# Kernel optimization log

Hardware: AMD Instinct MI355X
Metric: run time of the kernel (lower is better)

## Reference

```python
import jax, jax.numpy as jnp
import numpy as np

L_IN, L_FREQ, L_OUT = 128, 64, 64
C_IN, C_OUT, T_DIM = 64, 64, 256
SPIN = 1

# ---------- self-contained spin-weighted SHT (MW sampling), replacing s2fft ----------

def _mw_thetas(L, extended):
    n = 2 * L - 1 if extended else L
    return (2 * np.arange(n) + 1) * np.pi / (2 * L - 1)

def _wigner_d_stack(L, thetas, n):
    # d^l_{m,n}(theta) = <l,m| exp(-i theta Jy) |l,n>, computed via eigh of the
    # Hermitian angular-momentum operator Jy. Output (ntheta, L, 2L-1), m at col L-1+m.
    nth = len(thetas)
    out = np.zeros((nth, L, 2 * L - 1), dtype=np.float64)
    for l in range(abs(n), L):
        dim = 2 * l + 1
        m = np.arange(-l, l).astype(np.float64)
        ap = np.sqrt(l * (l + 1.0) - m * (m + 1.0))
        Jy = np.zeros((dim, dim), dtype=np.complex128)
        i = np.arange(dim - 1)
        Jy[i + 1, i] = -0.5j * ap
        Jy[i, i + 1] = 0.5j * ap
        lam, V = np.linalg.eigh(Jy)
        coeff = V * np.conj(V[l + n, :])[None, :]
        phases = np.exp(-1j * np.outer(lam, thetas))
        out[:, l, L - 1 - l:L + l] = (coeff @ phases).T.real
    return out

def _mw_quad_weights(L):
    # per-theta weights on the mirror-extended grid: q_t = (1/(2L-1)) sum_k w(k) e^{ik theta_t}
    # with w(k) = int_0^pi e^{ik t} sin(t) dt
    k = np.arange(-(L - 1), L)
    den = np.where(np.abs(k) == 1, 1, 1 - k * k).astype(np.float64)
    w = np.where(k % 2 == 0, 2.0 / den, 0.0).astype(np.complex128)
    w[k == 1] = 0.5j * np.pi
    w[k == -1] = -0.5j * np.pi
    th = _mw_thetas(L, True)
    return ((w[None, :] * np.exp(1j * np.outer(th, k))).sum(1) / (2 * L - 1)).real

# transform kernels are constants (built once at import, numpy)
_D_FWD = jnp.asarray(_wigner_d_stack(L_IN, _mw_thetas(L_IN, True), -SPIN) * _mw_quad_weights(L_IN)[:, None, None], jnp.float32)
_D_INV = jnp.asarray(_wigner_d_stack(L_OUT, _mw_thetas(L_OUT, False), -SPIN), jnp.float32)
_CL_IN = jnp.asarray(((-1.0) ** SPIN) * np.sqrt((2 * np.arange(L_IN) + 1) / (4 * np.pi)), jnp.float32)
_CL_OUT = jnp.asarray(((-1.0) ** SPIN) * np.sqrt((2 * np.arange(L_OUT) + 1) / (4 * np.pi)), jnp.float32)
_m_all = np.arange(-(L_IN - 1), L_IN)
_PARITY = jnp.asarray(np.where((_m_all + SPIN) % 2 == 0, 1.0, -1.0), jnp.float32)

def sht_forward(x):
    # x: (L_IN, 2*L_IN-1, C) real spatial -> flm: (L_IN, 2*L_IN-1, C) complex, m at L_IN-1+m
    nphi = 2 * L_IN - 1
    ftm = jnp.fft.fftshift(jnp.fft.fft(x, axis=1), axes=1) * (2 * jnp.pi / nphi)
    # mirror extension in theta with (-1)^(m+spin) parity (all channels at once)
    g_ext = jnp.concatenate([ftm, _PARITY[None, :, None] * ftm[::-1][1:]], axis=0)
    flm = jnp.einsum('tlm,tmc->lmc', _D_FWD, g_ext)
    return flm * _CL_IN[:, None, None]

def sht_inverse(flm):
    # flm: (L_OUT, 2*L_OUT-1, C) complex -> (L_OUT, 2*L_OUT-1, C) real spatial
    ftm = jnp.einsum('tlm,lmc->tmc', _D_INV, flm * _CL_OUT[:, None, None])
    return (jnp.fft.ifft(jnp.fft.ifftshift(ftm, axes=1), axis=1) * (2 * L_OUT - 1)).real

def resize_flm(flm, l_in, l_out):
    # centered truncation / zero-pad of (L, 2L-1, C) harmonic coefficients
    if l_out <= l_in:
        d = l_in - l_out
        return flm[:l_out, d:d + 2 * l_out - 1]
    d = l_out - l_in
    return jnp.pad(flm, ((0, d), (d, d), (0, 0)))

# ---------- inputs and parameters ----------

def setup_inputs():
    key = jax.random.key(0)
    ks = jax.random.split(key, 12)
    n = lambda i, shape, s: jax.random.normal(ks[i], shape, jnp.float32) * s
    return {
        'x': jax.random.normal(ks[0], (L_IN, 2 * L_IN - 1, C_IN), jnp.float32),
        't_emb': jax.random.normal(ks[1], (T_DIM,), jnp.float32),
        'spec_conv_w': n(2, (C_IN, C_OUT), (1.0 / C_IN) ** 0.5),
        'spec_conv_b': jnp.zeros((C_OUT,), jnp.float32),
        'spec_wr': n(3, (L_FREQ, C_IN, C_OUT), (0.5 / C_IN) ** 0.5),
        'spec_wi': n(4, (L_FREQ, C_IN, C_OUT), (0.5 / C_IN) ** 0.5),
        'spec_tr_w': n(5, (T_DIM, L_FREQ), (1.0 / T_DIM) ** 0.5),
        'spec_tr_b': jnp.zeros((L_FREQ,), jnp.float32),
        'spec_ti_w': n(6, (T_DIM, L_FREQ), (1.0 / T_DIM) ** 0.5),
        'spec_ti_b': jnp.zeros((L_FREQ,), jnp.float32),
        'spat_conv1_w': n(7, (C_IN, C_OUT), (1.0 / C_IN) ** 0.5),
        'spat_conv1_b': jnp.zeros((C_OUT,), jnp.float32),
        'spat_t_w': n(8, (T_DIM, 2 * C_OUT), (1.0 / T_DIM) ** 0.5),
        'spat_t_b': jnp.zeros((2 * C_OUT,), jnp.float32),
        'spat_weight': n(9, (C_OUT, C_OUT), 0.01),
        'spat_conv2_w': n(10, (C_OUT, C_OUT), (1.0 / C_OUT) ** 0.5),
        'spat_conv2_b': jnp.zeros((C_OUT,), jnp.float32),
        'ln_scale': jnp.ones((C_OUT,), jnp.float32),
        'ln_bias': jnp.zeros((C_OUT,), jnp.float32),
    }

def reference(x, t_emb, spec_conv_w, spec_conv_b, spec_wr, spec_wi, spec_tr_w, spec_tr_b, spec_ti_w, spec_ti_b, spat_conv1_w, spat_conv1_b, spat_t_w, spat_t_b, spat_weight, spat_conv2_w, spat_conv2_b, ln_scale, ln_bias):
    # ----- SphericalSpectralTimeConv branch -----
    flm = sht_forward(x)                                   # (L_IN, 2L_IN-1, C_IN) complex
    flm = resize_flm(flm, L_IN, L_FREQ)                    # (L_FREQ, 2L_FREQ-1, C_IN)
    conv_flm = jnp.einsum('lmi,io->lmo', flm, spec_conv_w) + spec_conv_b
    t_c = (t_emb @ spec_tr_w + spec_tr_b) + 1j * (t_emb @ spec_ti_w + spec_ti_b)   # (L_FREQ,)
    w = t_c[:, None, None] * (spec_wr + 1j * spec_wi)      # (L_FREQ, C_IN, C_OUT)
    flm = jnp.einsum('lmi,lio->lmo', flm, w) + conv_flm
    xs = sht_inverse(resize_flm(flm, L_FREQ, L_OUT))       # (L_OUT, 2L_OUT-1, C_OUT) real
    xs = xs / (jnp.linalg.norm(xs, axis=-1, keepdims=True) + 1e-6)
    # ----- SpatialTimeConv branch (path='down') -----
    h = jnp.einsum('lmi,io->lmo', x, spat_conv1_w) + spat_conv1_b
    t = t_emb @ spat_t_w + spat_t_b
    w_t, b_t = t[:C_OUT], t[C_OUT:]
    h = jnp.einsum('lmi,io->lmo', h, w_t[None, :] * spat_weight)
    h = sht_inverse(resize_flm(sht_forward(h), L_IN, L_OUT))
    h = jnp.einsum('lmi,io->lmo', h, spat_conv2_w) + spat_conv2_b + b_t
    # ----- combine: add, gelu, LayerNorm (eps=1e-6 over channels) -----
    y = jax.nn.gelu(xs + h)
    mu = jnp.mean(y, axis=-1, keepdims=True)
    var = jnp.var(y, axis=-1, keepdims=True)
    return (y - mu) * jax.lax.rsqrt(var + 1e-6) * ln_scale + ln_bias
```

## Files before the change

kernel.cpp:

```cpp
#include <hip/hip_runtime.h>
#include <math.h>

#define DPI 3.141592653589793238462643383279502884

__device__ __forceinline__ float wave_sum64(float v) {
#pragma unroll
  for (int off = 32; off > 0; off >>= 1) v += __shfl_xor(v, off, 64);
  return v;
}

__device__ __forceinline__ float gelu_tanh(float v) {
  float u = 0.7978845608028654f * (v + 0.044715f * v * v * v);
  return 0.5f * v * (1.0f + tanhf(u));
}

__global__ __launch_bounds__(256) void ct_setup(
    float* __restrict__ Deff, float* __restrict__ Dinv,
    float2* __restrict__ T255, float2* __restrict__ T127,
    const float* __restrict__ temb, const float* __restrict__ trw,
    const float* __restrict__ trb, const float* __restrict__ tiw,
    const float* __restrict__ tib, const float* __restrict__ stw,
    const float* __restrict__ stb, float* tcr, float* tci, float* tv) {
  int b = blockIdx.x;
  int tid = threadIdx.x;
  if (b >= 255) {
    if (b == 445) {
      if (tid < 64) {
        float ar = trb[tid], ai = tib[tid];
        for (int k = 0; k < 256; ++k) {
          float e = temb[k];
          ar = fmaf(e, trw[k * 64 + tid], ar);
          ai = fmaf(e, tiw[k * 64 + tid], ai);
        }
        tcr[tid] = ar; tci[tid] = ai;
      } else if (tid < 192) {
        int j = tid - 64;
        float a = stb[j];
        for (int k = 0; k < 256; ++k) a = fmaf(temb[k], stw[k * 128 + j], a);
        tv[j] = a;
      }
    } else {
      int id = (b - 255) * 256 + tid;
      if (id < 255 * 127) {
        int p = id / 127, mm = id % 127;
        double ang = 2.0 * DPI * (double)((mm - 63) * p) / 255.0;
        T255[id] = make_float2((float)cos(ang), (float)(-sin(ang)));
      }
      if (id < 127 * 127) {
        int mm = id / 127, p = id % 127;
        double ang = 2.0 * DPI * (double)((mm - 63) * p) / 127.0;
        T127[id] = make_float2((float)cos(ang), (float)sin(ang));
      }
    }
    return;
  }
  __shared__ double red[64];
  __shared__ float clf[64];
  int mode = (b < 128) ? 0 : 1;
  if (tid < 64)
    clf[tid] = (float)(-sqrt((2.0 * tid + 1.0) / (4.0 * DPI)));
  int t, mm;
  if (mode == 0) { t = b; mm = tid; }
  else { mm = b - 128; t = tid; }
  double denomN = (mode == 0) ? 255.0 : 127.0;
  double beta = (2.0 * t + 1.0) * DPI / denomN;
  float coeff;
  if (mode == 0) {
    if (tid < 63) {
      int k = 2 * (tid + 1);
      red[tid] = 8.0 * cos((double)k * beta) / (1.0 - (double)k * (double)k);
    } else if (tid == 63) {
      red[63] = 4.0;
    }
    __syncthreads();
    for (int s = 32; s > 0; s >>= 1) {
      if (tid < s) red[tid] += red[tid + s];
      __syncthreads();
    }
    double s = red[0] / 255.0;
    if (t == 127) s *= 0.5;
    coeff = (float)(s * (2.0 * DPI / 255.0));
    if (tid >= 127) return;
  } else {
    __syncthreads();
    coeff = 1.0f;
    if (tid >= 64) return;
  }
  int m = mm - 63;
  double cb = cos(beta);
  double ch = cos(0.5 * beta), sh = sin(0.5 * beta);
  int am = (m < 0) ? -m : m;
  int l0v = (am > 1) ? am : 1;
  double seed;
  if (m >= 1) {
    double j = (double)m;
    double K = exp(0.5 * (lgamma(2.0 * j + 1.0) - lgamma(j) - lgamma(j + 2.0)));
    double sgn = ((m + 1) & 1) ? -1.0 : 1.0;
    seed = sgn * K * pow(ch, j - 1.0) * pow(sh, j + 1.0);
  } else if (m <= -1) {
    double j = (double)(-m);
    double K = exp(0.5 * (lgamma(2.0 * j + 1.0) - lgamma(j) - lgamma(j + 2.0)));
    seed = K * pow(ch, j + 1.0) * pow(sh, j - 1.0);
  } else {
    seed = -sqrt(2.0) * sh * ch;
  }
  float dl = (float)seed, dm1 = 0.0f, S_cur = 0.0f;
  float cbf = (float)cb, mf = (float)m;
  for (int l = 0; l < 64; ++l) {
    float val = 0.0f;
    if (l >= l0v) {
      val = dl * coeff * clf[l];
      float Ld = (float)l, lp = Ld + 1.0f;
      float S_next = sqrtf((lp * lp - mf * mf) * (lp * lp - 1.0f));
      float num1 = (2.0f * Ld + 1.0f) * (Ld * lp * cbf + mf);
      float dn = (num1 * dl - lp * S_cur * dm1) / (Ld * S_next);
      dm1 = dl; dl = dn; S_cur = S_next;
    }
    if (mode == 0) Deff[((size_t)t * 127 + mm) * 64 + l] = val;
    else Dinv[((size_t)mm * 64 + l) * 64 + t] = val;
  }
}

__global__ void ct_AM(const float* __restrict__ cw, const float* __restrict__ wr,
                      const float* __restrict__ wi, const float* __restrict__ tcr,
                      const float* __restrict__ tci, const float* __restrict__ c1w,
                      const float* __restrict__ c1b, const float* __restrict__ sw,
                      const float* __restrict__ tv, const float* __restrict__ Deff,
                      float2* __restrict__ A2, float* __restrict__ Mm,
                      float* __restrict__ bias2, float* __restrict__ Sl) {
  int b = blockIdx.x, o = threadIdx.x;
  if (b < 64) {
    int l = b;
    float tr = tcr[l], ti = tci[l];
    for (int i = 0; i < 64; ++i) {
      int idx = (l * 64 + i) * 64 + o;
      float r = wr[idx], s = wi[idx];
      A2[idx] = make_float2(cw[i * 64 + o] + tr * r - ti * s, tr * s + ti * r);
    }
  } else if (b < 128) {
    int j = b - 64;
    float wt = tv[o];
    float acc = 0.f;
    for (int i = 0; i < 64; ++i) acc = fmaf(c1w[j * 64 + i], sw[i * 64 + o], acc);
    Mm[j * 64 + o] = wt * acc;
    if (j == 0) {
      float bb = 0.f;
      for (int i = 0; i < 64; ++i) bb = fmaf(c1b[i], sw[i * 64 + o], bb);
      bias2[o] = wt * bb;
    }
  } else {
    int l = o;
    float s = 0.f;
    for (int t = 0; t < 128; ++t) s += Deff[((size_t)t * 127 + 63) * 64 + l];
    Sl[l] = s;
  }
}

__global__ __launch_bounds__(256) void ct_dft(const float* __restrict__ x,
                                              const float2* __restrict__ T255,
                                              float* __restrict__ Are, float* __restrict__ Aim,
                                              float* __restrict__ Bre, float* __restrict__ Bim) {
  __shared__ float xs_[64][64];
  __shared__ float tsr[64][64], tsi[64][64];
  int t = blockIdx.x, mh = blockIdx.y, ph = blockIdx.z;
  float* ore = ph ? Bre : Are;
  float* oim = ph ? Bim : Aim;
  int pbase = ph * 128;
  int Ktot = ph ? 127 : 128;
  int tid = threadIdx.x;
  int cg = tid & 15, mg = tid >> 4;
  float accr[4][4], acci[4][4];
#pragma unroll
  for (int j = 0; j < 4; ++j)
#pragma unroll
    for (int q = 0; q < 4; ++q) { accr[j][q] = 0.f; acci[j][q] = 0.f; }
  for (int k0 = 0; k0 < Ktot; k0 += 64) {
    int kn = (Ktot - k0 < 64) ? Ktot - k0 : 64;
    __syncthreads();
    {
      int r = tid >> 2, c4 = (tid & 3) * 16;
      if (r < kn) {
        const float4* src = (const float4*)(x + ((size_t)t * 255 + pbase + k0 + r) * 64 + c4);
        float4* dst = (float4*)&xs_[r][c4];
        dst[0] = src[0]; dst[1] = src[1]; dst[2] = src[2]; dst[3] = src[3];
      }
    }
    for (int e = tid; e < 64 * 64; e += 256) {
      int r = e >> 6, mi = e & 63;
      if (r < kn) {
        int gcol = mh * 64 + mi; if (gcol > 126) gcol = 126;
        float2 tw = T255[(size_t)(pbase + k0 + r) * 127 + gcol];
        tsr[r][mi] = tw.x; tsi[r][mi] = tw.y;
      }
    }
    __syncthreads();
#pragma unroll 4
    for (int k = 0; k < kn; ++k) {
      float4 xv = *(const float4*)&xs_[k][cg * 4];
      float4 tr4 = *(const float4*)&tsr[k][mg * 4];
      float4 ti4 = *(const float4*)&tsi[k][mg * 4];
      float xv4[4] = {xv.x, xv.y, xv.z, xv.w};
      float trv[4] = {tr4.x, tr4.y, tr4.z, tr4.w};
      float tiv[4] = {ti4.x, ti4.y, ti4.z, ti4.w};
#pragma unroll
      for (int j = 0; j < 4; ++j)
#pragma unroll
        for (int q = 0; q < 4; ++q) {
          accr[j][q] = fmaf(xv4[q], trv[j], accr[j][q]);
          acci[j][q] = fmaf(xv4[q], tiv[j], acci[j][q]);
        }
    }
  }
#pragma unroll
  for (int j = 0; j < 4; ++j) {
    int gmm = mh * 64 + mg * 4 + j;
    if (gmm > 126) continue;
    size_t ob = ((size_t)t * 127 + gmm) * 64 + cg * 4;
    *(float4*)(ore + ob) = make_float4(accr[j][0], accr[j][1], accr[j][2], accr[j][3]);
    *(float4*)(oim + ob) = make_float4(acci[j][0], acci[j][1], acci[j][2], acci[j][3]);
  }
}

__global__ __launch_bounds__(256) void ct_projf(const float* __restrict__ Deff,
                                                const float* __restrict__ fAre,
                                                const float* __restrict__ fAim,
                                                const float* __restrict__ fBre,
                                                const float* __restrict__ fBim,
                                                float* __restrict__ flmA_re, float* __restrict__ flmA_im,
                                                float* __restrict__ flmB_re, float* __restrict__ flmB_im) {
  __shared__ float Dsh[64][32];
  __shared__ float fr_[64][64], fi_[64][64];
  int mm = blockIdx.x, lh = blockIdx.y, th = blockIdx.z;
  float* ore = th ? flmB_re : flmA_re;
  float* oim = th ? flmB_im : flmA_im;
  int tb = th * 64;
  int tid = threadIdx.x;
  int cg = tid & 15, lg = tid >> 4;
  for (int e = tid; e < 64 * 32; e += 256) {
    int r = e >> 5, li = e & 31;
    Dsh[r][li] = Deff[((size_t)(tb + r) * 127 + mm) * 64 + lh * 32 + li];
  }
  for (int e = tid; e < 64 * 64; e += 256) {
    int r = e >> 6, c = e & 63;
    size_t idx = ((size_t)(tb + r) * 127 + mm) * 64 + c;
    fr_[r][c] = fAre[idx] + fBre[idx];
    fi_[r][c] = fAim[idx] + fBim[idx];
  }
  __syncthreads();
  float ar[2][4], ai[2][4];
#pragma unroll
  for (int li = 0; li < 2; ++li)
#pragma unroll
    for (int q = 0; q < 4; ++q) { ar[li][q] = 0.f; ai[li][q] = 0.f; }
#pragma unroll 4
  for (int k = 0; k < 64; ++k) {
    float4 fr4 = *(const float4*)&fr_[k][cg * 4];
    float4 fi4 = *(const float4*)&fi_[k][cg * 4];
    float2 d2 = *(const float2*)&Dsh[k][lg * 2];
    float frv[4] = {fr4.x, fr4.y, fr4.z, fr4.w};
    float fiv[4] = {fi4.x, fi4.y, fi4.z, fi4.w};
    float dv[2] = {d2.x, d2.y};
#pragma unroll
    for (int li = 0; li < 2; ++li)
#pragma unroll
      for (int q = 0; q < 4; ++q) {
        ar[li][q] = fmaf(dv[li], frv[q], ar[li][q]);
        ai[li][q] = fmaf(dv[li], fiv[q], ai[li][q]);
      }
  }
#pragma unroll
  for (int li = 0; li < 2; ++li) {
    size_t row = ((size_t)mm * 64 + lh * 32 + lg * 2 + li) * 64 + cg * 4;
    *(float4*)(ore + row) = make_float4(ar[li][0], ar[li][1], ar[li][2], ar[li][3]);
    *(float4*)(oim + row) = make_float4(ai[li][0], ai[li][1], ai[li][2], ai[li][3]);
  }
}

__global__ __launch_bounds__(256) void ct_mix(const float* __restrict__ flmA_re,
                                              const float* __restrict__ flmA_im,
                                              const float* __restrict__ flmB_re,
                                              const float* __restrict__ flmB_im,
                                              const float2* __restrict__ A2,
                                              const float* __restrict__ Mm,
                                              const float* __restrict__ scb,
                                              const float* __restrict__ bias2,
                                              const float* __restrict__ Sl,
                                              float* __restrict__ s_re, float* __restrict__ s_im,
                                              float* __restrict__ h_re, float* __restrict__ h_im) {
  __shared__ float Ar_[64][32], Ai_[64][32], Msh[64][32];
  __shared__ float Br_[64][65], Bi_[64][65];
  int l = blockIdx.x, mh = blockIdx.y, oh = blockIdx.z;
  int tid = threadIdx.x;
  int og = tid & 15, mg = tid >> 4;
  for (int e = tid; e < 64 * 32; e += 256) {
    int r = e >> 5, oi = e & 31;
    float2 a = A2[((size_t)l * 64 + r) * 64 + oh * 32 + oi];
    Ar_[r][oi] = a.x; Ai_[r][oi] = a.y;
    Msh[r][oi] = Mm[r * 64 + oh * 32 + oi];
  }
  for (int e = tid; e < 64 * 64; e += 256) {
    int mi = e >> 6, i = e & 63;
    int gmm = mh * 64 + mi; if (gmm > 126) gmm = 126;
    size_t idx = ((size_t)gmm * 64 + l) * 64 + i;
    Br_[mi][i] = flmA_re[idx] + flmB_re[idx];
    Bi_[mi][i] = flmA_im[idx] + flmB_im[idx];
  }
  __syncthreads();
  int o0 = oh * 32 + og * 2;
  float b0[2] = {scb[o0], scb[o0 + 1]};
  float sr[4][2], si[4][2], hr[4][2], hi[4][2];
#pragma unroll
  for (int jm = 0; jm < 4; ++jm)
#pragma unroll
    for (int qo = 0; qo < 2; ++qo) {
      sr[jm][qo] = b0[qo]; si[jm][qo] = 0.f; hr[jm][qo] = 0.f; hi[jm][qo] = 0.f;
    }
#pragma unroll 4
  for (int k = 0; k < 64; ++k) {
    float2 ar2 = *(const float2*)&Ar_[k][og * 2];
    float2 ai2 = *(const float2*)&Ai_[k][og * 2];
    float2 mv2 = *(const float2*)&Msh[k][og * 2];
    float br4[4], bi4[4];
#pragma unroll
    for (int jm = 0; jm < 4; ++jm) {
      br4[jm] = Br_[mg * 4 + jm][k];
      bi4[jm] = Bi_[mg * 4 + jm][k];
    }
    float arv[2] = {ar2.x, ar2.y}, aiv[2] = {ai2.x, ai2.y}, mvv[2] = {mv2.x, mv2.y};
#pragma unroll
    for (int jm = 0; jm < 4; ++jm)
#pragma unroll
      for (int qo = 0; qo < 2; ++qo) {
        sr[jm][qo] = fmaf(br4[jm], arv[qo], sr[jm][qo]);
        sr[jm][qo] = fmaf(-bi4[jm], aiv[qo], sr[jm][qo]);
        si[jm][qo] = fmaf(br4[jm], aiv[qo], si[jm][qo]);
        si[jm][qo] = fmaf(bi4[jm], arv[qo], si[jm][qo]);
        hr[jm][qo] = fmaf(br4[jm], mvv[qo], hr[jm][qo]);
        hi[jm][qo] = fmaf(bi4[jm], mvv[qo], hi[jm][qo]);
      }
  }
  float Slv = Sl[l];
  float bb[2] = {bias2[o0], bias2[o0 + 1]};
#pragma unroll
  for (int jm = 0; jm < 4; ++jm) {
    int gmm = mh * 64 + mg * 4 + jm;
    if (gmm > 126) continue;
    if (gmm == 63) {
#pragma unroll
      for (int qo = 0; qo < 2; ++qo)
        hr[jm][qo] = fmaf(255.0f * Slv, bb[qo], hr[jm][qo]);
    }
    size_t row = ((size_t)gmm * 64 + l) * 64 + o0;
    *(float2*)(s_re + row) = make_float2(sr[jm][0], sr[jm][1]);
    *(float2*)(s_im + row) = make_float2(si[jm][0], si[jm][1]);
    *(float2*)(h_re + row) = make_float2(hr[jm][0], hr[jm][1]);
    *(float2*)(h_im + row) = make_float2(hi[jm][0], hi[jm][1]);
  }
}

__global__ __launch_bounds__(256) void ct_proji(const float* __restrict__ Dinv,
                                                const float* __restrict__ s_re,
                                                const float* __restrict__ s_im,
                                                const float* __restrict__ h_re,
                                                const float* __restrict__ h_im,
                                                float* __restrict__ fos_re, float* __restrict__ fos_im,
                                                float* __restrict__ foh_re, float* __restrict__ foh_im) {
  __shared__ float Dsh[64][64];
  __shared__ float Br_[64][32], Bi_[64][32];
  int mm = blockIdx.x, br = blockIdx.y, ch = blockIdx.z;
  const float* ire = br ? h_re : s_re;
  const float* iim = br ? h_im : s_im;
  float* ore = br ? foh_re : fos_re;
  float* oim = br ? foh_im : fos_im;
  int tid = threadIdx.x;
  int cg = tid & 15, tg = tid >> 4;
  for (int e = tid; e < 64 * 64; e += 256) {
    int r = e >> 6, tt = e & 63;
    Dsh[r][tt] = Dinv[((size_t)mm * 64 + r) * 64 + tt];
  }
  for (int e = tid; e < 64 * 32; e += 256) {
    int r = e >> 5, cc = e & 31;
    size_t idx = ((size_t)mm * 64 + r) * 64 + ch * 32 + cc;
    Br_[r][cc] = ire[idx];
    Bi_[r][cc] = iim[idx];
  }
  __syncthreads();
  float ar[4][2], ai[4][2];
#pragma unroll
  for (int j = 0; j < 4; ++j)
#pragma unroll
    for (int q = 0; q < 2; ++q) { ar[j][q] = 0.f; ai[j][q] = 0.f; }
#pragma unroll 4
  for (int k = 0; k < 64; ++k) {
    float4 d4 = *(const float4*)&Dsh[k][tg * 4];
    float2 fr2 = *(const float2*)&Br_[k][cg * 2];
    float2 fi2 = *(const float2*)&Bi_[k][cg * 2];
    float dv[4] = {d4.x, d4.y, d4.z, d4.w};
    float frv[2] = {fr2.x, fr2.y}, fiv[2] = {fi2.x, fi2.y};
#pragma unroll
    for (int j = 0; j < 4; ++j)
#pragma unroll
      for (int q = 0; q < 2; ++q) {
        ar[j][q] = fmaf(dv[j], frv[q], ar[j][q]);
        ai[j][q] = fmaf(dv[j], fiv[q], ai[j][q]);
      }
  }
#pragma unroll
  for (int j = 0; j < 4; ++j) {
    int t = tg * 4 + j;
    size_t ob = ((size_t)t * 127 + mm) * 64 + ch * 32 + cg * 2;
    *(float2*)(ore + ob) = make_float2(ar[j][0], ar[j][1]);
    *(float2*)(oim + ob) = make_float2(ai[j][0], ai[j][1]);
  }
}

__global__ __launch_bounds__(256) void ct_idft(const float2* __restrict__ T127,
                                               const float* __restrict__ fos_re,
                                               const float* __restrict__ fos_im,
                                               const float* __restrict__ foh_re,
                                               const float* __restrict__ foh_im,
                                               float* __restrict__ xsbA, float* __restrict__ xsbB,
                                               float* __restrict__ hsbA, float* __restrict__ hsbB) {
  __shared__ float Ar_[32][64], Ai_[32][64], Br_[32][64], Bi_[32][64];
  int t = blockIdx.x, br = blockIdx.y;
  int z = blockIdx.z;
  int ph = z >> 1, kh = z & 1;
  const float* fre = br ? foh_re : fos_re;
  const float* fim = br ? foh_im : fos_im;
  float* outp = br ? (kh ? hsbB : hsbA) : (kh ? xsbB : xsbA);
  int kbase = kh * 64;
  int Ktot = kh ? 63 : 64;
  int tid = threadIdx.x;
  int cg = tid & 15, pg = tid >> 4;
  float acc[4][4];
#pragma unroll
  for (int j = 0; j < 4; ++j)
#pragma unroll
    for (int q = 0; q < 4; ++q) acc[j][q] = 0.f;
  for (int k0 = 0; k0 < Ktot; k0 += 32) {
    int kn = (Ktot - k0 < 32) ? Ktot - k0 : 32;
    __syncthreads();
    for (int e = tid; e < 32 * 64; e += 256) {
      int r = e >> 6, j = e & 63;
      if (r < kn) {
        int gmm = kbase + k0 + r;
        int gp = ph * 64 + j; if (gp > 126) gp = 126;
        float2 tw = T127[(size_t)gmm * 127 + gp];
        Ar_[r][j] = tw.x; Ai_[r][j] = tw.y;
        size_t bidx = ((size_t)t * 127 + gmm) * 64 + j;
        Br_[r][j] = fre[bidx]; Bi_[r][j] = fim[bidx];
      }
    }
    __syncthreads();
#pragma unroll 4
    for (int k = 0; k < kn; ++k) {
      float4 a_r = *(const float4*)&Ar_[k][pg * 4];
      float4 a_i = *(const float4*)&Ai_[k][pg * 4];
      float4 b_r = *(const float4*)&Br_[k][cg * 4];
      float4 b_i = *(const float4*)&Bi_[k][cg * 4];
      float arv[4] = {a_r.x, a_r.y, a_r.z, a_r.w};
      float aiv[4] = {a_i.x, a_i.y, a_i.z, a_i.w};
      float brv[4] = {b_r.x, b_r.y, b_r.z, b_r.w};
      float biv[4] = {b_i.x, b_i.y, b_i.z, b_i.w};
#pragma unroll
      for (int j = 0; j < 4; ++j)
#pragma unroll
        for (int q = 0; q < 4; ++q) {
          acc[j][q] = fmaf(brv[q], arv[j], acc[j][q]);
          acc[j][q] = fmaf(biv[q], -aiv[j], acc[j][q]);
        }
    }
  }
#pragma unroll
  for (int j = 0; j < 4; ++j) {
    int gp = ph * 64 + pg * 4 + j;
    if (gp > 126) continue;
    *(float4*)(outp + ((size_t)t * 127 + gp) * 64 + cg * 4) =
        make_float4(acc[j][0], acc[j][1], acc[j][2], acc[j][3]);
  }
}

__global__ __launch_bounds__(256) void ct_fin(const float* __restrict__ xsbA,
                                              const float* __restrict__ xsbB,
                                              const float* __restrict__ hsbA,
                                              const float* __restrict__ hsbB,
                                              const float* __restrict__ c2w,
                                              const float* __restrict__ c2b,
                                              const float* __restrict__ tv,
                                              const float* __restrict__ lns,
                                              const float* __restrict__ lnb,
                                              float* __restrict__ out) {
  int w = threadIdx.x >> 6, lane = threadIdx.x & 63;
  size_t row = (size_t)blockIdx.x * 4 + w;
  size_t base = row * 64 + lane;
  float hv = hsbA[base] + hsbB[base];
  float xv = xsbA[base] + xsbB[base];
  float acc = c2b[lane] + tv[64 + lane];
#pragma unroll 16
  for (int i = 0; i < 64; ++i)
    acc = fmaf(__shfl(hv, i, 64), c2w[i * 64 + lane], acc);
  float ss = wave_sum64(xv * xv);
  xv = xv / (sqrtf(ss) + 1e-6f);
  float y = xv + acc;
  float g = gelu_tanh(y);
  float mu = wave_sum64(g) * (1.0f / 64.0f);
  float d = g - mu;
  float var = wave_sum64(d * d) * (1.0f / 64.0f);
  out[base] = d * rsqrtf(var + 1e-6f) * lns[lane] + lnb[lane];
}

extern "C" void kernel_launch(void* const* d_in, const int* in_sizes, int n_in,
                              void* d_out, int out_size, void* d_ws, size_t ws_size,
                              hipStream_t stream) {
  const float* x = (const float*)d_in[0];
  const float* temb = (const float*)d_in[1];
  const float* scw = (const float*)d_in[2];
  const float* scb = (const float*)d_in[3];
  const float* swr = (const float*)d_in[4];
  const float* swi = (const float*)d_in[5];
  const float* strw = (const float*)d_in[6];
  const float* strb = (const float*)d_in[7];
  const float* stiw = (const float*)d_in[8];
  const float* stib = (const float*)d_in[9];
  const float* c1w = (const float*)d_in[10];
  const float* c1b = (const float*)d_in[11];
  const float* stw = (const float*)d_in[12];
  const float* stb = (const float*)d_in[13];
  const float* sweight = (const float*)d_in[14];
  const float* c2w = (const float*)d_in[15];
  const float* c2b = (const float*)d_in[16];
  const float* lns = (const float*)d_in[17];
  const float* lnb = (const float*)d_in[18];
  float* out = (float*)d_out;

  char* base = (char*)d_ws;
  size_t off = 0;
  auto alloc = [&](size_t bytes) -> void* {
    void* p = base + off;
    off += (bytes + 255) & ~(size_t)255;
    return p;
  };
  float* tcr = (float*)alloc(64 * sizeof(float));
  float* tci = (float*)alloc(64 * sizeof(float));
  float* tv = (float*)alloc(128 * sizeof(float));
  float* Mm = (float*)alloc(4096 * sizeof(float));
  float* bias2 = (float*)alloc(64 * sizeof(float));
  float* Sl = (float*)alloc(64 * sizeof(float));
  float2* A2 = (float2*)alloc(262144 * sizeof(float2));
  float* Deff = (float*)alloc(1040384 * sizeof(float));
  float* Dinv = (float*)alloc(520192 * sizeof(float));
  float2* T255 = (float2*)alloc(32385 * sizeof(float2));
  float2* T127 = (float2*)alloc(16129 * sizeof(float2));
  float* ftmA_re = (float*)alloc(1040384 * sizeof(float));
  float* ftmA_im = (float*)alloc(1040384 * sizeof(float));
  float* ftmB_re = (float*)alloc(1040384 * sizeof(float));
  float* ftmB_im = (float*)alloc(1040384 * sizeof(float));
  float* flmA_re = (float*)alloc(520192 * sizeof(float));
  float* flmA_im = (float*)alloc(520192 * sizeof(float));
  float* flmB_re = (float*)alloc(520192 * sizeof(float));
  float* flmB_im = (float*)alloc(520192 * sizeof(float));
  if (off > ws_size) return;
  float* s_re = ftmA_re;
  float* s_im = ftmA_im;
  float* h_re = ftmB_re;
  float* h_im = ftmB_im;
  float* fos_re = Deff;
  float* fos_im = Deff + 520192;
  float* foh_re = flmA_re;
  float* foh_im = flmA_im;
  float* xsbA = flmB_re;
  float* xsbB = flmB_im;
  float* hsbA = ftmA_re;
  float* hsbB = ftmA_im;

  hipLaunchKernelGGL(ct_setup, dim3(446), dim3(256), 0, stream, Deff, Dinv, T255, T127,
                     temb, strw, strb, stiw, stib, stw, stb, tcr, tci, tv);
  hipLaunchKernelGGL(ct_AM, dim3(129), dim3(64), 0, stream, scw, swr, swi, tcr, tci,
                     c1w, c1b, sweight, tv, Deff, A2, Mm, bias2, Sl);
  hipLaunchKernelGGL(ct_dft, dim3(128, 2, 2), dim3(256), 0, stream, x, T255,
                     ftmA_re, ftmA_im, ftmB_re, ftmB_im);
  hipLaunchKernelGGL(ct_projf, dim3(127, 2, 2), dim3(256), 0, stream, Deff,
                     ftmA_re, ftmA_im, ftmB_re, ftmB_im,
                     flmA_re, flmA_im, flmB_re, flmB_im);
  hipLaunchKernelGGL(ct_mix, dim3(64, 2, 2), dim3(256), 0, stream,
                     flmA_re, flmA_im, flmB_re, flmB_im, A2, Mm, scb, bias2, Sl,
                     s_re, s_im, h_re, h_im);
  hipLaunchKernelGGL(ct_proji, dim3(127, 2, 2), dim3(256), 0, stream, Dinv,
                     s_re, s_im, h_re, h_im, fos_re, fos_im, foh_re, foh_im);
  hipLaunchKernelGGL(ct_idft, dim3(64, 2, 4), dim3(256), 0, stream, T127,
                     fos_re, fos_im, foh_re, foh_im, xsbA, xsbB, hsbA, hsbB);
  hipLaunchKernelGGL(ct_fin, dim3(2032), dim3(256), 0, stream, xsbA, xsbB, hsbA, hsbB,
                     c2w, c2b, tv, lns, lnb, out);
}
```

Baseline: 206.9 us.

## Fuse all pipeline stages into one persistent cooperative kernel with grid syncs

Replaces the sequence of eight kernel launches with a single cooperative kernel of 512 blocks. Each block loops over the work items of every stage and uses grid-wide barriers between stages. It also computes DFT twiddles inline with __sincosf instead of reading precomputed tables, and spreads the small setup reductions across threads. The aim is to remove per-launch overhead and the tail gaps between dependent stages, at the cost of grid-sync latency, a fixed block count that may underfill some stages, and lower twiddle precision; the old launch path is kept as a fallback if the cooperative launch fails.

```diff
diff --git a/kernel.cpp b/kernel.cpp
--- a/kernel.cpp
+++ b/kernel.cpp
@@ -1,5 +1,8 @@
 #include <hip/hip_runtime.h>
+#include <hip/hip_cooperative_groups.h>
 #include <math.h>
+
+namespace cg = cooperative_groups;
 
 #define DPI 3.141592653589793238462643383279502884
 
@@ -12,6 +15,519 @@
 __device__ __forceinline__ float gelu_tanh(float v) {
   float u = 0.7978845608028654f * (v + 0.044715f * v * v * v);
   return 0.5f * v * (1.0f + tanhf(u));
+}
+
+struct AllArgs {
+  const float *x, *temb, *scw, *scb, *swr, *swi, *strw, *strb, *stiw, *stib;
+  const float *c1w, *c1b, *stw, *stb, *sweight, *c2w, *c2b, *lns, *lnb;
+  float* out;
+  float* A2;
+  float* Mm;
+  float* bias2;
+  float* tv;
+  float* Deff;
+  float* Dinv;
+  float *ftmA_re, *ftmA_im, *ftmB_re, *ftmB_im;
+  float *flmA_re, *flmA_im, *flmB_re, *flmB_im;
+  float *s_re, *s_im, *h_re, *h_im;
+  float *fos_re, *fos_im, *foh_re, *foh_im;
+  float *xsbA, *xsbB, *hsbA, *hsbB;
+};
+
+#define CN255F ((float)(-2.0 * DPI / 255.0))
+#define CN127F ((float)(2.0 * DPI / 127.0))
+
+__device__ __forceinline__ void wigner_block(int b, int tid, const AllArgs& a, char* sm) {
+  double* red = (double*)sm;
+  float* clf = (float*)(sm + 512);
+  int mode = (b < 128) ? 0 : 1;
+  if (tid < 64) clf[tid] = (float)(-sqrt((2.0 * tid + 1.0) / (4.0 * DPI)));
+  int t, mm;
+  if (mode == 0) { t = b; mm = tid; }
+  else { mm = b - 128; t = tid; }
+  double denomN = (mode == 0) ? 255.0 : 127.0;
+  double beta = (2.0 * t + 1.0) * DPI / denomN;
+  float coeff = 1.0f;
+  if (mode == 0) {
+    if (tid < 63) {
+      int k = 2 * (tid + 1);
+      red[tid] = 8.0 * cos((double)k * beta) / (1.0 - (double)k * (double)k);
+    } else if (tid == 63) {
+      red[63] = 4.0;
+    }
+    __syncthreads();
+    for (int s = 32; s > 0; s >>= 1) {
+      if (tid < s) red[tid] += red[tid + s];
+      __syncthreads();
+    }
+    double s = red[0] / 255.0;
+    if (t == 127) s *= 0.5;
+    coeff = (float)(s * (2.0 * DPI / 255.0));
+  } else {
+    __syncthreads();
+  }
+  bool active = (mode == 0) ? (tid < 127) : (tid < 64);
+  if (!active) return;
+  int m = mm - 63;
+  double cb = cos(beta);
+  double ch = cos(0.5 * beta), sh = sin(0.5 * beta);
+  int am = (m < 0) ? -m : m;
+  int l0v = (am > 1) ? am : 1;
+  double seed;
+  if (m >= 1) {
+    double j = (double)m;
+    double K = exp(0.5 * (lgamma(2.0 * j + 1.0) - lgamma(j) - lgamma(j + 2.0)));
+    double sgn = ((m + 1) & 1) ? -1.0 : 1.0;
+    seed = sgn * K * pow(ch, j - 1.0) * pow(sh, j + 1.0);
+  } else if (m <= -1) {
+    double j = (double)(-m);
+    double K = exp(0.5 * (lgamma(2.0 * j + 1.0) - lgamma(j) - lgamma(j + 2.0)));
+    seed = K * pow(ch, j + 1.0) * pow(sh, j - 1.0);
+  } else {
+    seed = -sqrt(2.0) * sh * ch;
+  }
+  float dl = (float)seed, dm1 = 0.0f, S_cur = 0.0f;
+  float cbf = (float)cb, mf = (float)m;
+  for (int l = 0; l < 64; ++l) {
+    float val = 0.0f;
+    if (l >= l0v) {
+      val = dl * coeff * clf[l];
+      float Ld = (float)l, lp = Ld + 1.0f;
+      float S_next = sqrtf((lp * lp - mf * mf) * (lp * lp - 1.0f));
+      float num1 = (2.0f * Ld + 1.0f) * (Ld * lp * cbf + mf);
+      float dn = (num1 * dl - lp * S_cur * dm1) / (Ld * S_next);
+      dm1 = dl; dl = dn; S_cur = S_next;
+    }
+    if (mode == 0) a.Deff[((size_t)t * 127 + mm) * 64 + l] = val;
+    else a.Dinv[((size_t)mm * 64 + l) * 64 + t] = val;
+  }
+}
+
+__device__ __forceinline__ void a2_block(int l, int tid, const AllArgs& a, char* sm) {
+  float* redr = (float*)sm;
+  float* redi = (float*)(sm + 1024);
+  redr[tid] = a.temb[tid] * a.strw[tid * 64 + l];
+  redi[tid] = a.temb[tid] * a.stiw[tid * 64 + l];
+  __syncthreads();
+  for (int s = 128; s > 0; s >>= 1) {
+    if (tid < s) { redr[tid] += redr[tid + s]; redi[tid] += redi[tid + s]; }
+    __syncthreads();
+  }
+  float tr = redr[0] + a.strb[l], ti = redi[0] + a.stib[l];
+  int o = tid & 63, iq = tid >> 6;
+  float2* A2 = (float2*)a.A2;
+  for (int i = iq * 16; i < iq * 16 + 16; ++i) {
+    int idx = (l * 64 + i) * 64 + o;
+    float r = a.swr[idx], s2 = a.swi[idx];
+    A2[idx] = make_float2(a.scw[i * 64 + o] + tr * r - ti * s2, tr * s2 + ti * r);
+  }
+}
+
+__device__ __forceinline__ void m_block(int j, int tid, const AllArgs& a, char* sm) {
+  float* buf = (float*)sm;
+  float* tvsh = (float*)(sm + 1024);
+  int o = tid & 63, part = tid >> 6;
+  float p = 0.f;
+  for (int k = part * 64; k < part * 64 + 64; ++k) p = fmaf(a.temb[k], a.stw[k * 128 + o], p);
+  buf[part * 64 + o] = p;
+  __syncthreads();
+  if (part == 0) tvsh[o] = buf[o] + buf[64 + o] + buf[128 + o] + buf[192 + o] + a.stb[o];
+  __syncthreads();
+  float tvo = tvsh[o];
+  float q = 0.f;
+  for (int i = part * 16; i < part * 16 + 16; ++i)
+    q = fmaf(a.c1w[j * 64 + i], a.sweight[i * 64 + o], q);
+  __syncthreads();
+  buf[part * 64 + o] = q;
+  __syncthreads();
+  if (part == 0) a.Mm[j * 64 + o] = tvo * (buf[o] + buf[64 + o] + buf[128 + o] + buf[192 + o]);
+  if (j == 0) {
+    float bq = 0.f;
+    for (int i = part * 16; i < part * 16 + 16; ++i)
+      bq = fmaf(a.c1b[i], a.sweight[i * 64 + o], bq);
+    __syncthreads();
+    buf[part * 64 + o] = bq;
+    __syncthreads();
+    if (part == 0) a.bias2[o] = tvo * (buf[o] + buf[64 + o] + buf[128 + o] + buf[192 + o]);
+  }
+}
+
+__device__ __forceinline__ void tv_block(int tid, const AllArgs& a, char* sm) {
+  float* buf = (float*)sm;
+  int o = tid & 127, part = tid >> 7;
+  float p = 0.f;
+  for (int k = part * 128; k < part * 128 + 128; ++k)
+    p = fmaf(a.temb[k], a.stw[k * 128 + o], p);
+  buf[part * 128 + o] = p;
+  __syncthreads();
+  if (part == 0) a.tv[o] = buf[o] + buf[128 + o] + a.stb[o];
+}
+
+__device__ __forceinline__ void dft_block(int idx, int tid, const AllArgs& a, char* sm) {
+  float* xs_ = (float*)sm;
+  float* tsr = (float*)(sm + 16384);
+  float* tsi = (float*)(sm + 32768);
+  int t = idx >> 2, mh = (idx >> 1) & 1, ph = idx & 1;
+  float* ore = ph ? a.ftmB_re : a.ftmA_re;
+  float* oim = ph ? a.ftmB_im : a.ftmA_im;
+  int pbase = ph * 128;
+  int Ktot = ph ? 127 : 128;
+  int cg_ = tid & 15, mg = tid >> 4;
+  float accr[4][4], acci[4][4];
+#pragma unroll
+  for (int j = 0; j < 4; ++j)
+#pragma unroll
+    for (int q = 0; q < 4; ++q) { accr[j][q] = 0.f; acci[j][q] = 0.f; }
+  for (int k0 = 0; k0 < Ktot; k0 += 64) {
+    int kn = (Ktot - k0 < 64) ? Ktot - k0 : 64;
+    __syncthreads();
+    {
+      int r = tid >> 2, c4 = (tid & 3) * 16;
+      if (r < kn) {
+        const float4* src = (const float4*)(a.x + ((size_t)t * 255 + pbase + k0 + r) * 64 + c4);
+        float4* dst = (float4*)&xs_[r * 64 + c4];
+        dst[0] = src[0]; dst[1] = src[1]; dst[2] = src[2]; dst[3] = src[3];
+      }
+    }
+    for (int e = tid; e < 64 * 64; e += 256) {
+      int r = e >> 6, mi = e & 63;
+      if (r < kn) {
+        int gcol = mh * 64 + mi; if (gcol > 126) gcol = 126;
+        int p = pbase + k0 + r;
+        float ang = CN255F * (float)((gcol - 63) * p);
+        float sv, cv;
+        __sincosf(ang, &sv, &cv);
+        tsr[r * 64 + mi] = cv; tsi[r * 64 + mi] = sv;
+      }
+    }
+    __syncthreads();
+#pragma unroll 4
+    for (int k = 0; k < kn; ++k) {
+      float4 xv = *(const float4*)&xs_[k * 64 + cg_ * 4];
+      float4 tr4 = *(const float4*)&tsr[k * 64 + mg * 4];
+      float4 ti4 = *(const float4*)&tsi[k * 64 + mg * 4];
+      float xv4[4] = {xv.x, xv.y, xv.z, xv.w};
+      float trv[4] = {tr4.x, tr4.y, tr4.z, tr4.w};
+      float tiv[4] = {ti4.x, ti4.y, ti4.z, ti4.w};
+#pragma unroll
+      for (int j = 0; j < 4; ++j)
+#pragma unroll
+        for (int q = 0; q < 4; ++q) {
+          accr[j][q] = fmaf(xv4[q], trv[j], accr[j][q]);
+          acci[j][q] = fmaf(xv4[q], tiv[j], acci[j][q]);
+        }
+    }
+  }
+  __syncthreads();
+#pragma unroll
+  for (int j = 0; j < 4; ++j) {
+    int gmm = mh * 64 + mg * 4 + j;
+    if (gmm > 126) continue;
+    size_t ob = ((size_t)t * 127 + gmm) * 64 + cg_ * 4;
+    *(float4*)(ore + ob) = make_float4(accr[j][0], accr[j][1], accr[j][2], accr[j][3]);
+    *(float4*)(oim + ob) = make_float4(acci[j][0], acci[j][1], acci[j][2], acci[j][3]);
+  }
+}
+
+__device__ __forceinline__ void projf_block(int idx, int tid, const AllArgs& a, char* sm) {
+  float* Dsh = (float*)sm;
+  float* fr_ = (float*)(sm + 8192);
+  float* fi_ = (float*)(sm + 24576);
+  int mm = idx >> 2, lh = (idx >> 1) & 1, th = idx & 1;
+  float* ore = th ? a.flmB_re : a.flmA_re;
+  float* oim = th ? a.flmB_im : a.flmA_im;
+  int tb = th * 64;
+  int cg_ = tid & 15, lg = tid >> 4;
+  for (int e = tid; e < 64 * 32; e += 256) {
+    int r = e >> 5, li = e & 31;
+    Dsh[r * 32 + li] = a.Deff[((size_t)(tb + r) * 127 + mm) * 64 + lh * 32 + li];
+  }
+  for (int e = tid; e < 64 * 64; e += 256) {
+    int r = e >> 6, c = e & 63;
+    size_t idx2 = ((size_t)(tb + r) * 127 + mm) * 64 + c;
+    fr_[r * 64 + c] = a.ftmA_re[idx2] + a.ftmB_re[idx2];
+    fi_[r * 64 + c] = a.ftmA_im[idx2] + a.ftmB_im[idx2];
+  }
+  __syncthreads();
+  float ar[2][4], ai[2][4];
+#pragma unroll
+  for (int li = 0; li < 2; ++li)
+#pragma unroll
+    for (int q = 0; q < 4; ++q) { ar[li][q] = 0.f; ai[li][q] = 0.f; }
+#pragma unroll 4
+  for (int k = 0; k < 64; ++k) {
+    float4 fr4 = *(const float4*)&fr_[k * 64 + cg_ * 4];
+    float4 fi4 = *(const float4*)&fi_[k * 64 + cg_ * 4];
+    float2 d2 = *(const float2*)&Dsh[k * 32 + lg * 2];
+    float frv[4] = {fr4.x, fr4.y, fr4.z, fr4.w};
+    float fiv[4] = {fi4.x, fi4.y, fi4.z, fi4.w};
+    float dv[2] = {d2.x, d2.y};
+#pragma unroll
+    for (int li = 0; li < 2; ++li)
+#pragma unroll
+      for (int q = 0; q < 4; ++q) {
+        ar[li][q] = fmaf(dv[li], frv[q], ar[li][q]);
+        ai[li][q] = fmaf(dv[li], fiv[q], ai[li][q]);
+      }
+  }
+  __syncthreads();
+#pragma unroll
+  for (int li = 0; li < 2; ++li) {
+    size_t row = ((size_t)mm * 64 + lh * 32 + lg * 2 + li) * 64 + cg_ * 4;
+    *(float4*)(ore + row) = make_float4(ar[li][0], ar[li][1], ar[li][2], ar[li][3]);
+    *(float4*)(oim + row) = make_float4(ai[li][0], ai[li][1], ai[li][2], ai[li][3]);
+  }
+}
+
+__device__ __forceinline__ void mix_block(int idx, int tid, const AllArgs& a, char* sm) {
+  float* Ar_ = (float*)sm;
+  float* Ai_ = (float*)(sm + 8192);
+  float* Msh = (float*)(sm + 16384);
+  float* Br_ = (float*)(sm + 24576);
+  float* Bi_ = (float*)(sm + 41216);
+  int l = idx >> 2, mh = (idx >> 1) & 1, oh = idx & 1;
+  float slv;
+  {
+    float* rb = (float*)sm;
+    rb[tid] = (mh == 0 && tid < 128) ? a.Deff[((size_t)tid * 127 + 63) * 64 + l] : 0.f;
+    __syncthreads();
+    for (int s = 128; s > 0; s >>= 1) {
+      if (tid < s) rb[tid] += rb[tid + s];
+      __syncthreads();
+    }
+    slv = rb[0];
+    __syncthreads();
+  }
+  int og = tid & 15, mg = tid >> 4;
+  for (int e = tid; e < 64 * 32; e += 256) {
+    int r = e >> 5, oi = e & 31;
+    float2 av = ((const float2*)a.A2)[((size_t)l * 64 + r) * 64 + oh * 32 + oi];
+    Ar_[r * 32 + oi] = av.x; Ai_[r * 32 + oi] = av.y;
+    Msh[r * 32 + oi] = a.Mm[r * 64 + oh * 32 + oi];
+  }
+  for (int e = tid; e < 64 * 64; e += 256) {
+    int mi = e >> 6, i = e & 63;
+    int gmm = mh * 64 + mi; if (gmm > 126) gmm = 126;
+    size_t idx2 = ((size_t)gmm * 64 + l) * 64 + i;
+    Br_[mi * 65 + i] = a.flmA_re[idx2] + a.flmB_re[idx2];
+    Bi_[mi * 65 + i] = a.flmA_im[idx2] + a.flmB_im[idx2];
+  }
+  __syncthreads();
+  int o0 = oh * 32 + og * 2;
+  float b0[2] = {a.scb[o0], a.scb[o0 + 1]};
+  float sr[4][2], si[4][2], hr[4][2], hi[4][2];
+#pragma unroll
+  for (int jm = 0; jm < 4; ++jm)
+#pragma unroll
+    for (int qo = 0; qo < 2; ++qo) {
+      sr[jm][qo] = b0[qo]; si[jm][qo] = 0.f; hr[jm][qo] = 0.f; hi[jm][qo] = 0.f;
+    }
+#pragma unroll 4
+  for (int k = 0; k < 64; ++k) {
+    float2 ar2 = *(const float2*)&Ar_[k * 32 + og * 2];
+    float2 ai2 = *(const float2*)&Ai_[k * 32 + og * 2];
+    float2 mv2 = *(const float2*)&Msh[k * 32 + og * 2];
+    float br4[4], bi4[4];
+#pragma unroll
+    for (int jm = 0; jm < 4; ++jm) {
+      br4[jm] = Br_[(mg * 4 + jm) * 65 + k];
+      bi4[jm] = Bi_[(mg * 4 + jm) * 65 + k];
+    }
+    float arv[2] = {ar2.x, ar2.y}, aiv[2] = {ai2.x, ai2.y}, mvv[2] = {mv2.x, mv2.y};
+#pragma unroll
+    for (int jm = 0; jm < 4; ++jm)
+#pragma unroll
+      for (int qo = 0; qo < 2; ++qo) {
+        sr[jm][qo] = fmaf(br4[jm], arv[qo], sr[jm][qo]);
+        sr[jm][qo] = fmaf(-bi4[jm], aiv[qo], sr[jm][qo]);
+        si[jm][qo] = fmaf(br4[jm], aiv[qo], si[jm][qo]);
+        si[jm][qo] = fmaf(bi4[jm], arv[qo], si[jm][qo]);
+        hr[jm][qo] = fmaf(br4[jm], mvv[qo], hr[jm][qo]);
+        hi[jm][qo] = fmaf(bi4[jm], mvv[qo], hi[jm][qo]);
+      }
+  }
+  float bb[2] = {a.bias2[o0], a.bias2[o0 + 1]};
+  __syncthreads();
+#pragma unroll
+  for (int jm = 0; jm < 4; ++jm) {
+    int gmm = mh * 64 + mg * 4 + jm;
+    if (gmm > 126) continue;
+    if (gmm == 63) {
+#pragma unroll
+      for (int qo = 0; qo < 2; ++qo)
+        hr[jm][qo] = fmaf(255.0f * slv, bb[qo], hr[jm][qo]);
+    }
+    size_t row = ((size_t)gmm * 64 + l) * 64 + o0;
+    *(float2*)(a.s_re + row) = make_float2(sr[jm][0], sr[jm][1]);
+    *(float2*)(a.s_im + row) = make_float2(si[jm][0], si[jm][1]);
+    *(float2*)(a.h_re + row) = make_float2(hr[jm][0], hr[jm][1]);
+    *(float2*)(a.h_im + row) = make_float2(hi[jm][0], hi[jm][1]);
+  }
+}
+
+__device__ __forceinline__ void proji_block(int idx, int tid, const AllArgs& a, char* sm) {
+  float* Dsh = (float*)sm;
+  float* Br_ = (float*)(sm + 16384);
+  float* Bi_ = (float*)(sm + 24576);
+  int mm = idx >> 2, br = (idx >> 1) & 1, ch = idx & 1;
+  const float* ire = br ? a.h_re : a.s_re;
+  const float* iim = br ? a.h_im : a.s_im;
+  float* ore = br ? a.foh_re : a.fos_re;
+  float* oim = br ? a.foh_im : a.fos_im;
+  int cg_ = tid & 15, tg = tid >> 4;
+  for (int e = tid; e < 64 * 64; e += 256) {
+    int r = e >> 6, tt = e & 63;
+    Dsh[r * 64 + tt] = a.Dinv[((size_t)mm * 64 + r) * 64 + tt];
+  }
+  for (int e = tid; e < 64 * 32; e += 256) {
+    int r = e >> 5, cc = e & 31;
+    size_t idx2 = ((size_t)mm * 64 + r) * 64 + ch * 32 + cc;
+    Br_[r * 32 + cc] = ire[idx2];
+    Bi_[r * 32 + cc] = iim[idx2];
+  }
+  __syncthreads();
+  float ar[4][2], ai[4][2];
+#pragma unroll
+  for (int j = 0; j < 4; ++j)
+#pragma unroll
+    for (int q = 0; q < 2; ++q) { ar[j][q] = 0.f; ai[j][q] = 0.f; }
+#pragma unroll 4
+  for (int k = 0; k < 64; ++k) {
+    float4 d4 = *(const float4*)&Dsh[k * 64 + tg * 4];
+    float2 fr2 = *(const float2*)&Br_[k * 32 + cg_ * 2];
+    float2 fi2 = *(const float2*)&Bi_[k * 32 + cg_ * 2];
+    float dv[4] = {d4.x, d4.y, d4.z, d4.w};
+    float frv[2] = {fr2.x, fr2.y}, fiv[2] = {fi2.x, fi2.y};
+#pragma unroll
+    for (int j = 0; j < 4; ++j)
+#pragma unroll
+      for (int q = 0; q < 2; ++q) {
+        ar[j][q] = fmaf(dv[j], frv[q], ar[j][q]);
+        ai[j][q] = fmaf(dv[j], fiv[q], ai[j][q]);
+      }
+  }
+  __syncthreads();
+#pragma unroll
+  for (int j = 0; j < 4; ++j) {
+    int t = tg * 4 + j;
+    size_t ob = ((size_t)t * 127 + mm) * 64 + ch * 32 + cg_ * 2;
+    *(float2*)(ore + ob) = make_float2(ar[j][0], ar[j][1]);
+    *(float2*)(oim + ob) = make_float2(ai[j][0], ai[j][1]);
+  }
+}
+
+__device__ __forceinline__ void idft_block(int idx, int tid, const AllArgs& a, char* sm) {
+  float* Ar_ = (float*)sm;
+  float* Ai_ = (float*)(sm + 8192);
+  float* Br_ = (float*)(sm + 16384);
+  float* Bi_ = (float*)(sm + 24576);
+  int t = idx >> 3, br = (idx >> 2) & 1, z = idx & 3;
+  int ph = z >> 1, kh = z & 1;
+  const float* fre = br ? a.foh_re : a.fos_re;
+  const float* fim = br ? a.foh_im : a.fos_im;
+  float* outp = br ? (kh ? a.hsbB : a.hsbA) : (kh ? a.xsbB : a.xsbA);
+  int kbase = kh * 64;
+  int Ktot = kh ? 63 : 64;
+  int cg_ = tid & 15, pg = tid >> 4;
+  float acc[4][4];
+#pragma unroll
+  for (int j = 0; j < 4; ++j)
+#pragma unroll
+    for (int q = 0; q < 4; ++q) acc[j][q] = 0.f;
+  for (int k0 = 0; k0 < Ktot; k0 += 32) {
+    int kn = (Ktot - k0 < 32) ? Ktot - k0 : 32;
+    __syncthreads();
+    for (int e = tid; e < 32 * 64; e += 256) {
+      int r = e >> 6, j = e & 63;
+      if (r < kn) {
+        int gmm = kbase + k0 + r;
+        int gp = ph * 64 + j; if (gp > 126) gp = 126;
+        float ang = CN127F * (float)((gmm - 63) * gp);
+        float sv, cv;
+        __sincosf(ang, &sv, &cv);
+        Ar_[r * 64 + j] = cv; Ai_[r * 64 + j] = sv;
+        size_t bidx = ((size_t)t * 127 + gmm) * 64 + j;
+        Br_[r * 64 + j] = fre[bidx]; Bi_[r * 64 + j] = fim[bidx];
+      }
+    }
+    __syncthreads();
+#pragma unroll 4
+    for (int k = 0; k < kn; ++k) {
+      float4 a_r = *(const float4*)&Ar_[k * 64 + pg * 4];
+      float4 a_i = *(const float4*)&Ai_[k * 64 + pg * 4];
+      float4 b_r = *(const float4*)&Br_[k * 64 + cg_ * 4];
+      float4 b_i = *(const float4*)&Bi_[k * 64 + cg_ * 4];
+      float arv[4] = {a_r.x, a_r.y, a_r.z, a_r.w};
+      float aiv[4] = {a_i.x, a_i.y, a_i.z, a_i.w};
+      float brv[4] = {b_r.x, b_r.y, b_r.z, b_r.w};
+      float biv[4] = {b_i.x, b_i.y, b_i.z, b_i.w};
+#pragma unroll
+      for (int j = 0; j < 4; ++j)
+#pragma unroll
+        for (int q = 0; q < 4; ++q) {
+          acc[j][q] = fmaf(brv[q], arv[j], acc[j][q]);
+          acc[j][q] = fmaf(biv[q], -aiv[j], acc[j][q]);
+        }
+    }
+  }
+  __syncthreads();
+#pragma unroll
+  for (int j = 0; j < 4; ++j) {
+    int gp = ph * 64 + pg * 4 + j;
+    if (gp > 126) continue;
+    *(float4*)(outp + ((size_t)t * 127 + gp) * 64 + cg_ * 4) =
+        make_float4(acc[j][0], acc[j][1], acc[j][2], acc[j][3]);
+  }
+}
+
+__device__ __forceinline__ void fin_block(int idx, int tid, const AllArgs& a) {
+  int w = tid >> 6, lane = tid & 63;
+  float cbv = a.c2b[lane] + a.tv[64 + lane];
+  float lnsv = a.lns[lane], lnbv = a.lnb[lane];
+#pragma unroll
+  for (int rr = 0; rr < 4; ++rr) {
+    size_t row = (size_t)idx * 16 + rr * 4 + w;
+    size_t base2 = row * 64 + lane;
+    float hv = a.hsbA[base2] + a.hsbB[base2];
+    float xv = a.xsbA[base2] + a.xsbB[base2];
+    float acc = cbv;
+#pragma unroll 16
+    for (int i = 0; i < 64; ++i)
+      acc = fmaf(__shfl(hv, i, 64), a.c2w[i * 64 + lane], acc);
+    float ss = wave_sum64(xv * xv);
+    xv = xv / (sqrtf(ss) + 1e-6f);
+    float y = xv + acc;
+    float g = gelu_tanh(y);
+    float mu = wave_sum64(g) * (1.0f / 64.0f);
+    float d = g - mu;
+    float var = wave_sum64(d * d) * (1.0f / 64.0f);
+    a.out[base2] = d * rsqrtf(var + 1e-6f) * lnsv + lnbv;
+  }
+}
+
+__global__ __launch_bounds__(256, 2) void ct_all(AllArgs a) {
+  cg::grid_group grid = cg::this_grid();
+  __shared__ __align__(16) char sm[57856];
+  int tid = threadIdx.x;
+  int nb = gridDim.x;
+  for (int vb = blockIdx.x; vb < 896; vb += nb) {
+    if (vb < 255) wigner_block(vb, tid, a, sm);
+    else if (vb < 319) a2_block(vb - 255, tid, a, sm);
+    else if (vb < 383) m_block(vb - 319, tid, a, sm);
+    else if (vb < 384) tv_block(tid, a, sm);
+    else dft_block(vb - 384, tid, a, sm);
+    __syncthreads();
+  }
+  grid.sync();
+  for (int vb = blockIdx.x; vb < 508; vb += nb) { projf_block(vb, tid, a, sm); __syncthreads(); }
+  grid.sync();
+  for (int vb = blockIdx.x; vb < 256; vb += nb) { mix_block(vb, tid, a, sm); __syncthreads(); }
+  grid.sync();
+  for (int vb = blockIdx.x; vb < 508; vb += nb) { proji_block(vb, tid, a, sm); __syncthreads(); }
+  grid.sync();
+  for (int vb = blockIdx.x; vb < 512; vb += nb) { idft_block(vb, tid, a, sm); __syncthreads(); }
+  grid.sync();
+  for (int vb = blockIdx.x; vb < 508; vb += nb) fin_block(vb, tid, a);
 }
 
 __global__ __launch_bounds__(256) void ct_setup(
@@ -35,9 +551,9 @@
         tcr[tid] = ar; tci[tid] = ai;
       } else if (tid < 192) {
         int j = tid - 64;
-        float a = stb[j];
-        for (int k = 0; k < 256; ++k) a = fmaf(temb[k], stw[k * 128 + j], a);
-        tv[j] = a;
+        float aa = stb[j];
+        for (int k = 0; k < 256; ++k) aa = fmaf(temb[k], stw[k * 128 + j], aa);
+        tv[j] = aa;
       }
     } else {
       int id = (b - 255) * 256 + tid;
@@ -57,8 +573,7 @@
   __shared__ double red[64];
   __shared__ float clf[64];
   int mode = (b < 128) ? 0 : 1;
-  if (tid < 64)
-    clf[tid] = (float)(-sqrt((2.0 * tid + 1.0) / (4.0 * DPI)));
+  if (tid < 64) clf[tid] = (float)(-sqrt((2.0 * tid + 1.0) / (4.0 * DPI)));
   int t, mm;
   if (mode == 0) { t = b; mm = tid; }
   else { mm = b - 128; t = tid; }
@@ -156,10 +671,10 @@
   }
 }
 
-__global__ __launch_bounds__(256) void ct_dft(const float* __restrict__ x,
-                                              const float2* __restrict__ T255,
-                                              float* __restrict__ Are, float* __restrict__ Aim,
-                                              float* __restrict__ Bre, float* __restrict__ Bim) {
+__global__ __launch_bounds__(256) void ct_dft_fb(const float* __restrict__ x,
+                                                 const float2* __restrict__ T255,
+                                                 float* __restrict__ Are, float* __restrict__ Aim,
+                                                 float* __restrict__ Bre, float* __restrict__ Bim) {
   __shared__ float xs_[64][64];
   __shared__ float tsr[64][64], tsi[64][64];
   int t = blockIdx.x, mh = blockIdx.y, ph = blockIdx.z;
@@ -168,7 +683,7 @@
   int pbase = ph * 128;
   int Ktot = ph ? 127 : 128;
   int tid = threadIdx.x;
-  int cg = tid & 15, mg = tid >> 4;
+  int cg_ = tid & 15, mg = tid >> 4;
   float accr[4][4], acci[4][4];
 #pragma unroll
   for (int j = 0; j < 4; ++j)
@@ -196,7 +711,7 @@
     __syncthreads();
 #pragma unroll 4
     for (int k = 0; k < kn; ++k) {
-      float4 xv = *(const float4*)&xs_[k][cg * 4];
+      float4 xv = *(const float4*)&xs_[k][cg_ * 4];
       float4 tr4 = *(const float4*)&tsr[k][mg * 4];
       float4 ti4 = *(const float4*)&tsi[k][mg * 4];
       float xv4[4] = {xv.x, xv.y, xv.z, xv.w};
@@ -215,19 +730,19 @@
   for (int j = 0; j < 4; ++j) {
     int gmm = mh * 64 + mg * 4 + j;
     if (gmm > 126) continue;
-    size_t ob = ((size_t)t * 127 + gmm) * 64 + cg * 4;
+    size_t ob = ((size_t)t * 127 + gmm) * 64 + cg_ * 4;
     *(float4*)(ore + ob) = make_float4(accr[j][0], accr[j][1], accr[j][2], accr[j][3]);
     *(float4*)(oim + ob) = make_float4(acci[j][0], acci[j][1], acci[j][2], acci[j][3]);
   }
 }
 
-__global__ __launch_bounds__(256) void ct_projf(const float* __restrict__ Deff,
-                                                const float* __restrict__ fAre,
-                                                const float* __restrict__ fAim,
-                                                const float* __restrict__ fBre,
-                                                const float* __restrict__ fBim,
-                                                float* __restrict__ flmA_re, float* __restrict__ flmA_im,
-                                                float* __restrict__ flmB_re, float* __restrict__ flmB_im) {
+__global__ __launch_bounds__(256) void ct_projf_fb(const float* __restrict__ Deff,
+                                                   const float* __restrict__ fAre,
+                                                   const float* __restrict__ fAim,
+                                                   const float* __restrict__ fBre,
+                                                   const float* __restrict__ fBim,
+                                                   float* __restrict__ flmA_re, float* __restrict__ flmA_im,
+                                                   float* __restrict__ flmB_re, float* __restrict__ flmB_im) {
   __shared__ float Dsh[64][32];
   __shared__ float fr_[64][64], fi_[64][64];
   int mm = blockIdx.x, lh = blockIdx.y, th = blockIdx.z;
@@ -235,7 +750,7 @@
   float* oim = th ? flmB_im : flmA_im;
   int tb = th * 64;
   int tid = threadIdx.x;
-  int cg = tid & 15, lg = tid >> 4;
+  int cg_ = tid & 15, lg = tid >> 4;
   for (int e = tid; e < 64 * 32; e += 256) {
     int r = e >> 5, li = e & 31;
     Dsh[r][li] = Deff[((size_t)(tb + r) * 127 + mm) * 64 + lh * 32 + li];
@@ -254,8 +769,8 @@
     for (int q = 0; q < 4; ++q) { ar[li][q] = 0.f; ai[li][q] = 0.f; }
 #pragma unroll 4
   for (int k = 0; k < 64; ++k) {
-    float4 fr4 = *(const float4*)&fr_[k][cg * 4];
-    float4 fi4 = *(const float4*)&fi_[k][cg * 4];
+    float4 fr4 = *(const float4*)&fr_[k][cg_ * 4];
+    float4 fi4 = *(const float4*)&fi_[k][cg_ * 4];
     float2 d2 = *(const float2*)&Dsh[k][lg * 2];
     float frv[4] = {fr4.x, fr4.y, fr4.z, fr4.w};
     float fiv[4] = {fi4.x, fi4.y, fi4.z, fi4.w};
@@ -270,23 +785,23 @@
   }
 #pragma unroll
   for (int li = 0; li < 2; ++li) {
-    size_t row = ((size_t)mm * 64 + lh * 32 + lg * 2 + li) * 64 + cg * 4;
+    size_t row = ((size_t)mm * 64 + lh * 32 + lg * 2 + li) * 64 + cg_ * 4;
     *(float4*)(ore + row) = make_float4(ar[li][0], ar[li][1], ar[li][2], ar[li][3]);
     *(float4*)(oim + row) = make_float4(ai[li][0], ai[li][1], ai[li][2], ai[li][3]);
   }
 }
 
-__global__ __launch_bounds__(256) void ct_mix(const float* __restrict__ flmA_re,
-                                              const float* __restrict__ flmA_im,
-                                              const float* __restrict__ flmB_re,
-                                              const float* __restrict__ flmB_im,
-                                              const float2* __restrict__ A2,
-                                              const float* __restrict__ Mm,
-                                              const float* __restrict__ scb,
-                                              const float* __restrict__ bias2,
-                                              const float* __restrict__ Sl,
-                                              float* __restrict__ s_re, float* __restrict__ s_im,
-                                              float* __restrict__ h_re, float* __restrict__ h_im) {
+__global__ __launch_bounds__(256) void ct_mix_fb(const float* __restrict__ flmA_re,
+                                                 const float* __restrict__ flmA_im,
+                                                 const float* __restrict__ flmB_re,
+                                                 const float* __restrict__ flmB_im,
+                                                 const float2* __restrict__ A2,
+                                                 const float* __restrict__ Mm,
+                                                 const float* __restrict__ scb,
+                                                 const float* __restrict__ bias2,
+                                                 const float* __restrict__ Sl,
+                                                 float* __restrict__ s_re, float* __restrict__ s_im,
+                                                 float* __restrict__ h_re, float* __restrict__ h_im) {
   __shared__ float Ar_[64][32], Ai_[64][32], Msh[64][32];
   __shared__ float Br_[64][65], Bi_[64][65];
   int l = blockIdx.x, mh = blockIdx.y, oh = blockIdx.z;
@@ -294,8 +809,8 @@
   int og = tid & 15, mg = tid >> 4;
   for (int e = tid; e < 64 * 32; e += 256) {
     int r = e >> 5, oi = e & 31;
-    float2 a = A2[((size_t)l * 64 + r) * 64 + oh * 32 + oi];
-    Ar_[r][oi] = a.x; Ai_[r][oi] = a.y;
+    float2 aa = A2[((size_t)l * 64 + r) * 64 + oh * 32 + oi];
+    Ar_[r][oi] = aa.x; Ai_[r][oi] = aa.y;
     Msh[r][oi] = Mm[r * 64 + oh * 32 + oi];
   }
   for (int e = tid; e < 64 * 64; e += 256) {
@@ -358,13 +873,13 @@
   }
 }
 
-__global__ __launch_bounds__(256) void ct_proji(const float* __restrict__ Dinv,
-                                                const float* __restrict__ s_re,
-                                                const float* __restrict__ s_im,
-                                                const float* __restrict__ h_re,
-                                                const float* __restrict__ h_im,
-                                                float* __restrict__ fos_re, float* __restrict__ fos_im,
-                                                float* __restrict__ foh_re, float* __restrict__ foh_im) {
+__global__ __launch_bounds__(256) void ct_proji_fb(const float* __restrict__ Dinv,
+                                                   const float* __restrict__ s_re,
+                                                   const float* __restrict__ s_im,
+                                                   const float* __restrict__ h_re,
+                                                   const float* __restrict__ h_im,
+                                                   float* __restrict__ fos_re, float* __restrict__ fos_im,
+                                                   float* __restrict__ foh_re, float* __restrict__ foh_im) {
   __shared__ float Dsh[64][64];
   __shared__ float Br_[64][32], Bi_[64][32];
   int mm = blockIdx.x, br = blockIdx.y, ch = blockIdx.z;
@@ -373,7 +888,7 @@
   float* ore = br ? foh_re : fos_re;
   float* oim = br ? foh_im : fos_im;
   int tid = threadIdx.x;
-  int cg = tid & 15, tg = tid >> 4;
+  int cg_ = tid & 15, tg = tid >> 4;
   for (int e = tid; e < 64 * 64; e += 256) {
     int r = e >> 6, tt = e & 63;
     Dsh[r][tt] = Dinv[((size_t)mm * 64 + r) * 64 + tt];
@@ -393,8 +908,8 @@
 #pragma unroll 4
   for (int k = 0; k < 64; ++k) {
     float4 d4 = *(const float4*)&Dsh[k][tg * 4];
-    float2 fr2 = *(const float2*)&Br_[k][cg * 2];
-    float2 fi2 = *(const float2*)&Bi_[k][cg * 2];
+    float2 fr2 = *(const float2*)&Br_[k][cg_ * 2];
+    float2 fi2 = *(const float2*)&Bi_[k][cg_ * 2];
     float dv[4] = {d4.x, d4.y, d4.z, d4.w};
     float frv[2] = {fr2.x, fr2.y}, fiv[2] = {fi2.x, fi2.y};
 #pragma unroll
@@ -408,19 +923,19 @@
 #pragma unroll
   for (int j = 0; j < 4; ++j) {
     int t = tg * 4 + j;
-    size_t ob = ((size_t)t * 127 + mm) * 64 + ch * 32 + cg * 2;
+    size_t ob = ((size_t)t * 127 + mm) * 64 + ch * 32 + cg_ * 2;
     *(float2*)(ore + ob) = make_float2(ar[j][0], ar[j][1]);
     *(float2*)(oim + ob) = make_float2(ai[j][0], ai[j][1]);
   }
 }
 
-__global__ __launch_bounds__(256) void ct_idft(const float2* __restrict__ T127,
-                                               const float* __restrict__ fos_re,
-                                               const float* __restrict__ fos_im,
-                                               const float* __restrict__ foh_re,
-                                               const float* __restrict__ foh_im,
-                                               float* __restrict__ xsbA, float* __restrict__ xsbB,
-                                               float* __restrict__ hsbA, float* __restrict__ hsbB) {
+__global__ __launch_bounds__(256) void ct_idft_fb(const float2* __restrict__ T127,
+                                                  const float* __restrict__ fos_re,
+                                                  const float* __restrict__ fos_im,
+                                                  const float* __restrict__ foh_re,
+                                                  const float* __restrict__ foh_im,
+                                                  float* __restrict__ xsbA, float* __restrict__ xsbB,
+                                                  float* __restrict__ hsbA, float* __restrict__ hsbB) {
   __shared__ float Ar_[32][64], Ai_[32][64], Br_[32][64], Bi_[32][64];
   int t = blockIdx.x, br = blockIdx.y;
   int z = blockIdx.z;
@@ -431,7 +946,7 @@
   int kbase = kh * 64;
   int Ktot = kh ? 63 : 64;
   int tid = threadIdx.x;
-  int cg = tid & 15, pg = tid >> 4;
+  int cg_ = tid & 15, pg = tid >> 4;
   float acc[4][4];
 #pragma unroll
   for (int j = 0; j < 4; ++j)
@@ -456,8 +971,8 @@
     for (int k = 0; k < kn; ++k) {
       float4 a_r = *(const float4*)&Ar_[k][pg * 4];
       float4 a_i = *(const float4*)&Ai_[k][pg * 4];
-      float4 b_r = *(const float4*)&Br_[k][cg * 4];
-      float4 b_i = *(const float4*)&Bi_[k][cg * 4];
+      float4 b_r = *(const float4*)&Br_[k][cg_ * 4];
+      float4 b_i = *(const float4*)&Bi_[k][cg_ * 4];
       float arv[4] = {a_r.x, a_r.y, a_r.z, a_r.w};
       float aiv[4] = {a_i.x, a_i.y, a_i.z, a_i.w};
       float brv[4] = {b_r.x, b_r.y, b_r.z, b_r.w};
@@ -475,21 +990,21 @@
   for (int j = 0; j < 4; ++j) {
     int gp = ph * 64 + pg * 4 + j;
     if (gp > 126) continue;
-    *(float4*)(outp + ((size_t)t * 127 + gp) * 64 + cg * 4) =
+    *(float4*)(outp + ((size_t)t * 127 + gp) * 64 + cg_ * 4) =
         make_float4(acc[j][0], acc[j][1], acc[j][2], acc[j][3]);
   }
 }
 
-__global__ __launch_bounds__(256) void ct_fin(const float* __restrict__ xsbA,
-                                              const float* __restrict__ xsbB,
-                                              const float* __restrict__ hsbA,
-                                              const float* __restrict__ hsbB,
-                                              const float* __restrict__ c2w,
-                                              const float* __restrict__ c2b,
-                                              const float* __restrict__ tv,
-                                              const float* __restrict__ lns,
-                                              const float* __restrict__ lnb,
-                                              float* __restrict__ out) {
+__global__ __launch_bounds__(256) void ct_fin_fb(const float* __restrict__ xsbA,
+                                                 const float* __restrict__ xsbB,
+                                                 const float* __restrict__ hsbA,
+                                                 const float* __restrict__ hsbB,
+                                                 const float* __restrict__ c2w,
+                                                 const float* __restrict__ c2b,
+                                                 const float* __restrict__ tv,
+                                                 const float* __restrict__ lns,
+                                                 const float* __restrict__ lnb,
+                                                 float* __restrict__ out) {
   int w = threadIdx.x >> 6, lane = threadIdx.x & 63;
   size_t row = (size_t)blockIdx.x * 4 + w;
   size_t base = row * 64 + lane;
@@ -573,22 +1088,41 @@
   float* hsbA = ftmA_re;
   float* hsbB = ftmA_im;
 
+  AllArgs ha;
+  ha.x = x; ha.temb = temb; ha.scw = scw; ha.scb = scb; ha.swr = swr; ha.swi = swi;
+  ha.strw = strw; ha.strb = strb; ha.stiw = stiw; ha.stib = stib;
+  ha.c1w = c1w; ha.c1b = c1b; ha.stw = stw; ha.stb = stb; ha.sweight = sweight;
+  ha.c2w = c2w; ha.c2b = c2b; ha.lns = lns; ha.lnb = lnb;
+  ha.out = out;
+  ha.A2 = (float*)A2; ha.Mm = Mm; ha.bias2 = bias2; ha.tv = tv;
+  ha.Deff = Deff; ha.Dinv = Dinv;
+  ha.ftmA_re = ftmA_re; ha.ftmA_im = ftmA_im; ha.ftmB_re = ftmB_re; ha.ftmB_im = ftmB_im;
+  ha.flmA_re = flmA_re; ha.flmA_im = flmA_im; ha.flmB_re = flmB_re; ha.flmB_im = flmB_im;
+  ha.s_re = s_re; ha.s_im = s_im; ha.h_re = h_re; ha.h_im = h_im;
+  ha.fos_re = fos_re; ha.fos_im = fos_im; ha.foh_re = foh_re; ha.foh_im = foh_im;
+  ha.xsbA = xsbA; ha.xsbB = xsbB; ha.hsbA = hsbA; ha.hsbB = hsbB;
+
+  void* kargs[] = {(void*)&ha};
+  hipError_t err = hipLaunchCooperativeKernel(reinterpret_cast<void*>(&ct_all),
+                                              dim3(512), dim3(256), kargs, 0, stream);
+  if (err == hipSuccess) return;
+
   hipLaunchKernelGGL(ct_setup, dim3(446), dim3(256), 0, stream, Deff, Dinv, T255, T127,
                      temb, strw, strb, stiw, stib, stw, stb, tcr, tci, tv);
   hipLaunchKernelGGL(ct_AM, dim3(129), dim3(64), 0, stream, scw, swr, swi, tcr, tci,
                      c1w, c1b, sweight, tv, Deff, A2, Mm, bias2, Sl);
-  hipLaunchKernelGGL(ct_dft, dim3(128, 2, 2), dim3(256), 0, stream, x, T255,
+  hipLaunchKernelGGL(ct_dft_fb, dim3(128, 2, 2), dim3(256), 0, stream, x, T255,
                      ftmA_re, ftmA_im, ftmB_re, ftmB_im);
-  hipLaunchKernelGGL(ct_projf, dim3(127, 2, 2), dim3(256), 0, stream, Deff,
+  hipLaunchKernelGGL(ct_projf_fb, dim3(127, 2, 2), dim3(256), 0, stream, Deff,
                      ftmA_re, ftmA_im, ftmB_re, ftmB_im,
                      flmA_re, flmA_im, flmB_re, flmB_im);
-  hipLaunchKernelGGL(ct_mix, dim3(64, 2, 2), dim3(256), 0, stream,
+  hipLaunchKernelGGL(ct_mix_fb, dim3(64, 2, 2), dim3(256), 0, stream,
                      flmA_re, flmA_im, flmB_re, flmB_im, A2, Mm, scb, bias2, Sl,
                      s_re, s_im, h_re, h_im);
-  hipLaunchKernelGGL(ct_proji, dim3(127, 2, 2), dim3(256), 0, stream, Dinv,
+  hipLaunchKernelGGL(ct_proji_fb, dim3(127, 2, 2), dim3(256), 0, stream, Dinv,
                      s_re, s_im, h_re, h_im, fos_re, fos_im, foh_re, foh_im);
-  hipLaunchKernelGGL(ct_idft, dim3(64, 2, 4), dim3(256), 0, stream, T127,
+  hipLaunchKernelGGL(ct_idft_fb, dim3(64, 2, 4), dim3(256), 0, stream, T127,
                      fos_re, fos_im, foh_re, foh_im, xsbA, xsbB, hsbA, hsbB);
-  hipLaunchKernelGGL(ct_fin, dim3(2032), dim3(256), 0, stream, xsbA, xsbB, hsbA, hsbB,
+  hipLaunchKernelGGL(ct_fin_fb, dim3(2032), dim3(256), 0, stream, xsbA, xsbB, hsbA, hsbB,
                      c2w, c2b, tv, lns, lnb, out);
 }
```

New measurement: 544.7 us. 2.63x slower.
